# Kernel tuning notes

Measured on AMD Instinct MI355X. Metric: run time of the kernel, lower is better.

The kernel has to match this reference:

```python
import jax, jax.numpy as jnp
import numpy as np

B, L, H, P = 4, 4096, 1024, 256


def _bin_op(ei, ej):
    A_i, Bu_i = ei
    A_j, Bu_j = ej
    return (A_j * A_i, A_j * Bu_i + Bu_j)


def _s5(x, log_real, imag, B_real, B_imag, C_real, C_imag, D, log_Delta):
    Lam = jax.lax.complex(-jnp.exp(log_real), imag)                 # [P]
    B_tilde = jax.lax.complex(B_real, B_imag)                        # [P,H]
    C_tilde = jax.lax.complex(C_real, C_imag)                        # [H,P]
    Delta = jnp.exp(log_Delta)                                       # [P]
    Lambda_bar = jnp.exp(Lam * Delta)                                # [P]
    Lam_safe = jnp.where(jnp.abs(Lam) < 1e-6,
                         jnp.full_like(Lam, 1e-6), Lam)
    B_bar = ((Lambda_bar - 1.0) / Lam_safe)[:, None] * B_tilde       # [P,H]
    Bu = x.astype(jnp.complex64) @ B_bar.T                           # [B,L,P]
    La = jnp.broadcast_to(Lambda_bar[None, None, :], Bu.shape)
    _, xs = jax.lax.associative_scan(_bin_op, (La, Bu), axis=1)      # [B,L,P]
    ys = jnp.real(xs @ C_tilde.T) + D * x                            # [B,L,H]
    return jax.nn.gelu(ys, approximate=False)


def setup_inputs() -> dict:
    key = jax.random.key(0)
    ks = jax.random.split(key, 17)
    std_b = 1.0 / H ** 0.5
    std_c = 1.0 / P ** 0.5
    d = {"x": jax.random.normal(ks[0], (B, L, H), dtype=jnp.float32)}
    for i, pfx in enumerate(["fwd", "bwd"]):
        o = 1 + 8 * i
        d[pfx + "_log_real"] = jax.random.normal(ks[o], (P,)) * 0.5
        d[pfx + "_imag"] = jax.random.normal(ks[o + 1], (P,))
        d[pfx + "_B_real"] = jax.random.normal(ks[o + 2], (P, H)) * std_b
        d[pfx + "_B_imag"] = jax.random.normal(ks[o + 3], (P, H)) * std_b
        d[pfx + "_C_real"] = jax.random.normal(ks[o + 4], (H, P)) * std_c
        d[pfx + "_C_imag"] = jax.random.normal(ks[o + 5], (H, P)) * std_c
        d[pfx + "_D"] = jnp.ones((H,), dtype=jnp.float32)
        d[pfx + "_log_Delta"] = jnp.zeros((P,), dtype=jnp.float32)
    return d


def reference(x,
              fwd_log_real, fwd_imag, fwd_B_real, fwd_B_imag,
              fwd_C_real, fwd_C_imag, fwd_D, fwd_log_Delta,
              bwd_log_real, bwd_imag, bwd_B_real, bwd_B_imag,
              bwd_C_real, bwd_C_imag, bwd_D, bwd_log_Delta):
    y_f = _s5(x, fwd_log_real, fwd_imag, fwd_B_real, fwd_B_imag,
              fwd_C_real, fwd_C_imag, fwd_D, fwd_log_Delta)
    x_flip = jnp.flip(x, axis=1)
    y_b = _s5(x_flip, bwd_log_real, bwd_imag, bwd_B_real, bwd_B_imag,
              bwd_C_real, bwd_C_imag, bwd_D, bwd_log_Delta)
    return y_f + jnp.flip(y_b, axis=1)
```

## Files before the change

### kernel.cpp

```cpp
#include <hip/hip_runtime.h>
#include <math.h>


typedef short bf16x8 __attribute__((ext_vector_type(8)));
typedef float f32x4 __attribute__((ext_vector_type(4)));
typedef unsigned short u16x8 __attribute__((ext_vector_type(8)));

__device__ __forceinline__ unsigned short f2bf(float f) {
  union { float f; unsigned int u; } v; v.f = f;
  unsigned int r = (v.u + 0x7FFFu + ((v.u >> 16) & 1u)) >> 16;
  return (unsigned short)r;
}
__device__ __forceinline__ float bf2f(unsigned short s) {
  union { unsigned int u; float f; } v; v.u = ((unsigned int)s) << 16;
  return v.f;
}
__device__ __forceinline__ float gelu_fast(float v) {
  const float u = 1.5957691216057308f * fmaf(0.044715f * v, v * v, v);
  return v / (1.f + __expf(-u));
}
__device__ __forceinline__ void gload16(const unsigned short* g, void* l) {
  __builtin_amdgcn_global_load_lds(
      (const __attribute__((address_space(1))) void*)g,
      (__attribute__((address_space(3))) void*)l, 16, 0, 0);
}

__global__ __launch_bounds__(256) void cast_prep_kernel(
    const float* __restrict__ x, unsigned short* __restrict__ xbf,
    const float* __restrict__ flr, const float* __restrict__ fim,
    const float* __restrict__ fBr, const float* __restrict__ fBi,
    const float* __restrict__ fCr, const float* __restrict__ fCi,
    const float* __restrict__ flD,
    const float* __restrict__ blr, const float* __restrict__ bim,
    const float* __restrict__ bBr, const float* __restrict__ bBi,
    const float* __restrict__ bCr, const float* __restrict__ bCi,
    const float* __restrict__ blD,
    unsigned short* __restrict__ W, unsigned short* __restrict__ CmT,
    float4* __restrict__ lamp) {
  const int tid = threadIdx.x;
  if (blockIdx.x < 8192) {
    const size_t i = (size_t)blockIdx.x * 256 + tid;
    const float4* xv = (const float4*)x;
    float4 a = xv[2 * i], b = xv[2 * i + 1];
    u16x8 r;
    r[0] = f2bf(a.x); r[1] = f2bf(a.y); r[2] = f2bf(a.z); r[3] = f2bf(a.w);
    r[4] = f2bf(b.x); r[5] = f2bf(b.y); r[6] = f2bf(b.z); r[7] = f2bf(b.w);
    *(u16x8*)(xbf + 8 * i) = r;
    return;
  }
  const int bid = blockIdx.x - 8192;
  if (bid < 512) {
    const int dir = bid >> 8, p = bid & 255;
    const float* lr_ = dir ? blr : flr;
    const float* im_ = dir ? bim : fim;
    const float* lD_ = dir ? blD : flD;
    const float* Br_ = dir ? bBr : fBr;
    const float* Bi_ = dir ? bBi : fBi;
    const float Lre = -expf(lr_[p]);
    const float Lim = im_[p];
    const float Dl = expf(lD_[p]);
    const float ar = Lre * Dl, ai = Lim * Dl;
    const float er = expf(ar);
    const float lre = er * cosf(ai), lim = er * sinf(ai);
    const float e64 = expf(64.f * ar);
    const float l64re = e64 * cosf(64.f * ai), l64im = e64 * sinf(64.f * ai);
    float sre = Lre, sim = Lim;
    if (sqrtf(Lre * Lre + Lim * Lim) < 1e-6f) { sre = 1e-6f; sim = 0.f; }
    const float den = sre * sre + sim * sim;
    const float fre = ((lre - 1.f) * sre + lim * sim) / den;
    const float fi2 = (lim * sre - (lre - 1.f) * sim) / den;
    if (tid == 0) lamp[dir * 256 + p] = make_float4(lre, lim, l64re, l64im);
    const size_t rowR = (size_t)(dir * 512 + 2 * p) * 1024;
    const size_t rowI = rowR + 1024;
    for (int h = tid; h < 1024; h += 256) {
      const float Br = Br_[p * 1024 + h], Bi = Bi_[p * 1024 + h];
      W[rowR + h] = f2bf(fre * Br - fi2 * Bi);
      W[rowI + h] = f2bf(fre * Bi + fi2 * Br);
    }
  } else {
    const int h = bid - 512;
    for (int k = tid; k < 1024; k += 256) {
      const int dir = k >> 9, within = k & 511;
      const int p = within >> 1, comp = within & 1;
      const float* C = comp ? (dir ? bCi : fCi) : (dir ? bCr : fCr);
      float v = C[(size_t)h * 256 + p];
      if (comp) v = -v;
      CmT[(size_t)h * 1024 + k] = f2bf(v);
    }
  }
}

#define G256_STAGE(BUF, KT, APTR, BPTR)                                        \
  {                                                                            \
    const int k0 = (KT) << 6;                                                  \
    _Pragma("unroll") for (int i = 0; i < 4; ++i) {                            \
      const int r = (i << 6) + tr;                                             \
      const int o = ((BUF) << 15) + (i << 13) + (tid << 4);                    \
      gload16(APTR + (size_t)(m0 + r) * 1024 + (k0 + csw), (char*)As + o);     \
      gload16(BPTR + (size_t)(n0 + r) * 1024 + (k0 + csw), (char*)Bs + o);     \
    }                                                                          \
  }

#define PIPE_PUBLISH8()                                                        \
  asm volatile("s_waitcnt vmcnt(8)" ::: "memory");                             \
  __builtin_amdgcn_sched_barrier(0);                                           \
  __builtin_amdgcn_s_barrier();                                                \
  __builtin_amdgcn_sched_barrier(0);

#define PIPE_CLOSE()                                                           \
  __builtin_amdgcn_sched_barrier(0);                                           \
  __builtin_amdgcn_s_barrier();                                                \
  __builtin_amdgcn_sched_barrier(0);

#define G1_COMPUTE(BUF, ACC)                                                   \
  {                                                                            \
    const int bo = (BUF) << 14;                            \
    bf16x8 bF[4][2];                                                           \
    _Pragma("unroll") for (int n4 = 0; n4 < 4; ++n4)                           \
        _Pragma("unroll") for (int kk2 = 0; kk2 < 2; ++kk2) {                  \
      const int row = (wn << 6) + (n4 << 4) + fr;                              \
      bF[n4][kk2] =                                                            \
          *(const bf16x8*)&Bs[bo + row * 64 + (((kk2 << 5) + ks) ^ sw)];       \
    }                                                                          \
    _Pragma("unroll") for (int ph = 0; ph < 4; ++ph) {                         \
      bf16x8 aF[2][2];                                                         \
      _Pragma("unroll") for (int mf2 = 0; mf2 < 2; ++mf2)                      \
          _Pragma("unroll") for (int kk2 = 0; kk2 < 2; ++kk2) {                \
        const int row = (wm << 7) + (((ph << 1) + mf2) << 4) + fr;             \
        aF[mf2][kk2] =                                                         \
            *(const bf16x8*)&As[bo + row * 64 + (((kk2 << 5) + ks) ^ sw)];     \
      }                                                                        \
      __builtin_amdgcn_s_setprio(1);                                           \
      _Pragma("unroll") for (int mf2 = 0; mf2 < 2; ++mf2)                      \
          _Pragma("unroll") for (int n4 = 0; n4 < 4; ++n4)                     \
              _Pragma("unroll") for (int kk2 = 0; kk2 < 2; ++kk2)              \
                  ACC[(ph << 1) + mf2][n4] =                                   \
                      __builtin_amdgcn_mfma_f32_16x16x32_bf16(                 \
                          aF[mf2][kk2], bF[n4][kk2], ACC[(ph << 1) + mf2][n4], \
                          0, 0, 0);                                            \
      __builtin_amdgcn_s_setprio(0);                                           \
    }                                                                          \
  }

__global__ __launch_bounds__(512, 2) void gemm1_kernel(
    const unsigned short* __restrict__ xbf, const unsigned short* __restrict__ W,
    unsigned short* __restrict__ Zb) {
  __shared__ unsigned short As[2 * 256 * 64];
  __shared__ unsigned short Bs[2 * 256 * 64];
  const int tid = threadIdx.x;
  const int lane = tid & 63;
  const int w = tid >> 6;
  const int wm = w >> 2, wn = w & 3;
  const int fr = lane & 15;
  const int ks = (lane >> 4) << 3;
  const int sw = (fr & 7) << 3;
  const int tr = tid >> 3;
  const int csw = ((tid & 7) ^ (tr & 7)) << 3;
  const int bsw = ((blockIdx.x & 7) << 5) + (blockIdx.x >> 3);
  const int nt = bsw & 3, mt = bsw >> 2;
  const int m0 = mt << 8, n0 = nt << 8;

  f32x4 acc[8][4] = {};

  G256_STAGE(0, 0, xbf, W);
  int cur = 0;
  for (int kt = 0; kt < 15; ++kt) {
    G256_STAGE(cur ^ 1, kt + 1, xbf, W);
    PIPE_PUBLISH8();
    G1_COMPUTE(cur, acc);
    PIPE_CLOSE();
    cur ^= 1;
  }
  __syncthreads();
  G1_COMPUTE(cur, acc);

  const int rb = (lane >> 4) << 2;
#pragma unroll
  for (int mf = 0; mf < 8; ++mf)
#pragma unroll
    for (int n4 = 0; n4 < 4; ++n4) {
      const size_t gn = n0 + (wn << 6) + (n4 << 4) + fr;
#pragma unroll
      for (int r = 0; r < 4; ++r) {
        const size_t gm = m0 + (wm << 7) + (mf << 4) + rb + r;
        Zb[gm * 1024 + gn] = f2bf(acc[mf][n4][r]);
      }
    }
}

__global__ __launch_bounds__(256) void scanP_kernel(
    const unsigned int* __restrict__ Zp, const float4* __restrict__ lamp,
    float2* __restrict__ part) {
  const int p = threadIdx.x;
  const int k = blockIdx.x & 63;
  const int s = blockIdx.x >> 6;
  const int dir = s & 1, b = s >> 1;
  const float4 lp = lamp[dir * 256 + p];
  const float lre = lp.x, lim = lp.y;
  const size_t col = (size_t)dir * 256 + p;
  const size_t mbase = (size_t)b * 4096 + (size_t)k * 64;
  float sre = 0.f, sim = 0.f;
  if (dir == 0) {
    for (int i = 0; i < 64; ++i) {
      const unsigned int u = Zp[(mbase + i) * 512 + col];
      const float nr = fmaf(lre, sre, fmaf(-lim, sim, bf2f((unsigned short)u)));
      const float ni = fmaf(lre, sim, fmaf(lim, sre, bf2f((unsigned short)(u >> 16))));
      sre = nr; sim = ni;
    }
  } else {
    for (int i = 63; i >= 0; --i) {
      const unsigned int u = Zp[(mbase + i) * 512 + col];
      const float nr = fmaf(lre, sre, fmaf(-lim, sim, bf2f((unsigned short)u)));
      const float ni = fmaf(lre, sim, fmaf(lim, sre, bf2f((unsigned short)(u >> 16))));
      sre = nr; sim = ni;
    }
  }
  part[(size_t)(s * 64 + k) * 256 + p] = make_float2(sre, sim);
}

__global__ __launch_bounds__(256) void scanF_kernel(
    const unsigned int* __restrict__ Zp, const float4* __restrict__ lamp,
    const float2* __restrict__ part, unsigned int* __restrict__ xsbf) {
  const int p = threadIdx.x;
  const int k = blockIdx.x & 63;
  const int s = blockIdx.x >> 6;
  const int dir = s & 1, b = s >> 1;
  const float4 lp = lamp[dir * 256 + p];
  const float lre = lp.x, lim = lp.y, wr64 = lp.z, wi64 = lp.w;
  const size_t col = (size_t)dir * 256 + p;
  const size_t mbase = (size_t)b * 4096 + (size_t)k * 64;

  float cr = 0.f, ci = 0.f, wr = 1.f, wi = 0.f;
  if (dir == 0) {
    for (int j = k - 1; j >= 0; --j) {
      const float2 S = part[(size_t)(s * 64 + j) * 256 + p];
      cr = fmaf(wr, S.x, fmaf(-wi, S.y, cr));
      ci = fmaf(wr, S.y, fmaf(wi, S.x, ci));
      const float t = wr * wr64 - wi * wi64;
      wi = wr * wi64 + wi * wr64; wr = t;
    }
  } else {
    for (int j = k + 1; j < 64; ++j) {
      const float2 S = part[(size_t)(s * 64 + j) * 256 + p];
      cr = fmaf(wr, S.x, fmaf(-wi, S.y, cr));
      ci = fmaf(wr, S.y, fmaf(wi, S.x, ci));
      const float t = wr * wr64 - wi * wi64;
      wi = wr * wi64 + wi * wr64; wr = t;
    }
  }

  float sre = cr, sim = ci;
  if (dir == 0) {
    for (int i = 0; i < 64; ++i) {
      const size_t idx = (mbase + i) * 512 + col;
      const unsigned int u = Zp[idx];
      const float nr = fmaf(lre, sre, fmaf(-lim, sim, bf2f((unsigned short)u)));
      const float ni = fmaf(lre, sim, fmaf(lim, sre, bf2f((unsigned short)(u >> 16))));
      sre = nr; sim = ni;
      xsbf[idx] = (unsigned int)f2bf(sre) | ((unsigned int)f2bf(sim) << 16);
    }
  } else {
    for (int i = 63; i >= 0; --i) {
      const size_t idx = (mbase + i) * 512 + col;
      const unsigned int u = Zp[idx];
      const float nr = fmaf(lre, sre, fmaf(-lim, sim, bf2f((unsigned short)u)));
      const float ni = fmaf(lre, sim, fmaf(lim, sre, bf2f((unsigned short)(u >> 16))));
      sre = nr; sim = ni;
      xsbf[idx] = (unsigned int)f2bf(sre) | ((unsigned int)f2bf(sim) << 16);
    }
  }
}

#define GEMM_STAGE(BUF, KT, APTR, BPTR)                                        \
  {                                                                            \
    const int k0 = (KT) << 6;                                                  \
    _Pragma("unroll") for (int i = 0; i < 4; ++i) {                            \
      const int r = (i << 5) + tr;                                             \
      const int o = ((BUF) << 14) + (i << 12) + (tid << 4);                    \
      gload16(APTR + (size_t)(m0 + r) * 1024 + (k0 + csw), (char*)As + o);     \
      gload16(BPTR + (size_t)(n0 + r) * 1024 + (k0 + csw), (char*)Bs + o);     \
    }                                                                          \
  }

#define GEMM_COMPUTE(BUF, ACC)                                                 \
  {                                                                            \
    const int bo = (BUF) << 13;               \
    _Pragma("unroll") for (int kk = 0; kk < 64; kk += 32) {                    \
      bf16x8 af[4], bf_[4];                                                    \
      _Pragma("unroll") for (int m4 = 0; m4 < 4; ++m4) {                       \
        const int row = (wm << 6) + (m4 << 4) + fr;                            \
        af[m4] = *(const bf16x8*)&As[bo + row * 64 + ((kk + ks) ^ sw)];        \
      }                                                                        \
      _Pragma("unroll") for (int n4 = 0; n4 < 4; ++n4) {                       \
        const int row = (wn << 6) + (n4 << 4) + fr;                            \
        bf_[n4] = *(const bf16x8*)&Bs[bo + row * 64 + ((kk + ks) ^ sw)];       \
      }                                                                        \
      _Pragma("unroll") for (int m4 = 0; m4 < 4; ++m4)                         \
          _Pragma("unroll") for (int n4 = 0; n4 < 4; ++n4)                     \
              ACC[m4][n4] = __builtin_amdgcn_mfma_f32_16x16x32_bf16(           \
                  af[m4], bf_[n4], ACC[m4][n4], 0, 0, 0);                      \
    }                                                                          \
  }

__global__ __launch_bounds__(256, 2) void gemm2_kernel(
    const unsigned short* __restrict__ A2, const unsigned short* __restrict__ CmT,
    const unsigned short* __restrict__ xbf, const float* __restrict__ Df,
    const float* __restrict__ Db, float* __restrict__ out) {
  __shared__ unsigned short As[2 * 128 * 64];
  __shared__ unsigned short Bs[2 * 128 * 64];
  const int tid = threadIdx.x;
  const int lane = tid & 63;
  const int w = tid >> 6;
  const int wm = w >> 1, wn = w & 1;
  const int fr = lane & 15;
  const int ks = (lane >> 4) << 3;
  const int sw = (fr & 7) << 3;
  const int tr = tid >> 3;
  const int csw = ((tid & 7) ^ (tr & 7)) << 3;
  const int bsw = ((blockIdx.x & 7) << 7) + (blockIdx.x >> 3);
  const int nt = bsw & 7, mt = bsw >> 3;
  const int m0 = mt << 7, n0 = nt << 7;

  f32x4 accf[4][4] = {};
  f32x4 accb[4][4] = {};

  GEMM_STAGE(0, 0, A2, CmT);
  int cur = 0;
#pragma unroll
  for (int kt = 0; kt < 8; ++kt) {
    GEMM_STAGE(cur ^ 1, kt + 1, A2, CmT);
    PIPE_PUBLISH8();
    GEMM_COMPUTE(cur, accf);
    PIPE_CLOSE();
    cur ^= 1;
  }
#pragma unroll
  for (int kt = 8; kt < 15; ++kt) {
    GEMM_STAGE(cur ^ 1, kt + 1, A2, CmT);
    PIPE_PUBLISH8();
    GEMM_COMPUTE(cur, accb);
    PIPE_CLOSE();
    cur ^= 1;
  }
  __syncthreads();
  GEMM_COMPUTE(cur, accb);

  const int rb = (lane >> 4) << 2;
#pragma unroll
  for (int n4 = 0; n4 < 4; ++n4) {
    const size_t gn = n0 + (wn << 6) + (n4 << 4) + fr;
    const float dfv = Df[gn], dbv = Db[gn];
#pragma unroll
    for (int m4 = 0; m4 < 4; ++m4) {
#pragma unroll
      for (int r = 0; r < 4; ++r) {
        const size_t gm = m0 + (wm << 6) + (m4 << 4) + rb + r;
        const float xv = bf2f(xbf[gm * 1024 + gn]);
        out[gm * 1024 + gn] = gelu_fast(accf[m4][n4][r] + dfv * xv) +
                              gelu_fast(accb[m4][n4][r] + dbv * xv);
      }
    }
  }
}

extern "C" void kernel_launch(void* const* d_in, const int* in_sizes, int n_in,
                              void* d_out, int out_size, void* d_ws, size_t ws_size,
                              hipStream_t stream) {
  const float* x = (const float*)d_in[0];
  const float* flr = (const float*)d_in[1];
  const float* fim = (const float*)d_in[2];
  const float* fBr = (const float*)d_in[3];
  const float* fBi = (const float*)d_in[4];
  const float* fCr = (const float*)d_in[5];
  const float* fCi = (const float*)d_in[6];
  const float* fD  = (const float*)d_in[7];
  const float* flD = (const float*)d_in[8];
  const float* blr = (const float*)d_in[9];
  const float* bim = (const float*)d_in[10];
  const float* bBr = (const float*)d_in[11];
  const float* bBi = (const float*)d_in[12];
  const float* bCr = (const float*)d_in[13];
  const float* bCi = (const float*)d_in[14];
  const float* bD  = (const float*)d_in[15];
  const float* blD = (const float*)d_in[16];

  char* ws = (char*)d_ws;
  unsigned short* xbf  = (unsigned short*)(ws);
  unsigned short* W    = (unsigned short*)(ws + 33554432);
  unsigned short* CmT  = (unsigned short*)(ws + 35651584);
  unsigned short* Zb   = (unsigned short*)(ws + 37748736);
  unsigned short* xsbf = (unsigned short*)(ws + 71303168);
  float4*         lamp = (float4*)(ws + 104857600);
  float2*         part = (float2*)(ws + 104865792);

  cast_prep_kernel<<<9728, 256, 0, stream>>>(
      x, xbf, flr, fim, fBr, fBi, fCr, fCi, flD,
      blr, bim, bBr, bBi, bCr, bCi, blD, W, CmT, lamp);
  gemm1_kernel<<<256, 512, 0, stream>>>(xbf, W, Zb);
  scanP_kernel<<<512, 256, 0, stream>>>((unsigned int*)Zb, lamp, part);
  scanF_kernel<<<512, 256, 0, stream>>>((unsigned int*)Zb, lamp, part,
                                        (unsigned int*)xsbf);
  gemm2_kernel<<<1024, 256, 0, stream>>>(xsbf, CmT, xbf, fD, bD, (float*)d_out);
}
```

Measured before the change: 145.4 us.

## Fuse chunk-local scan into GEMM1 epilogue and simplify scan fixup pass

Result: faster. 135.1 us, median of 2 (-7.1%).

```diff
diff --git a/kernel.cpp b/kernel.cpp
--- a/kernel.cpp
+++ b/kernel.cpp
@@ -144,9 +144,11 @@
 
 __global__ __launch_bounds__(512, 2) void gemm1_kernel(
     const unsigned short* __restrict__ xbf, const unsigned short* __restrict__ W,
-    unsigned short* __restrict__ Zb) {
-  __shared__ unsigned short As[2 * 256 * 64];
-  __shared__ unsigned short Bs[2 * 256 * 64];
+    unsigned int* __restrict__ Zp, const float4* __restrict__ lamp,
+    float2* __restrict__ part) {
+  __shared__ unsigned short LDS[4 * 256 * 64];
+  unsigned short* As = LDS;
+  unsigned short* Bs = LDS + 2 * 256 * 64;
   const int tid = threadIdx.x;
   const int lane = tid & 63;
   const int w = tid >> 6;
@@ -159,6 +161,7 @@
   const int bsw = ((blockIdx.x & 7) << 5) + (blockIdx.x >> 3);
   const int nt = bsw & 3, mt = bsw >> 2;
   const int m0 = mt << 8, n0 = nt << 8;
+  const int rb = (lane >> 4) << 2;
 
   f32x4 acc[8][4] = {};
 
@@ -174,48 +177,54 @@
   __syncthreads();
   G1_COMPUTE(cur, acc);
 
-  const int rb = (lane >> 4) << 2;
+  __syncthreads();
+  unsigned short (*SB)[256] = (unsigned short(*)[256])LDS;
 #pragma unroll
   for (int mf = 0; mf < 8; ++mf)
 #pragma unroll
     for (int n4 = 0; n4 < 4; ++n4) {
-      const size_t gn = n0 + (wn << 6) + (n4 << 4) + fr;
+      const int lc = (wn << 6) + (n4 << 4) + fr;
 #pragma unroll
       for (int r = 0; r < 4; ++r) {
-        const size_t gm = m0 + (wm << 7) + (mf << 4) + rb + r;
-        Zb[gm * 1024 + gn] = f2bf(acc[mf][n4][r]);
+        const int lr = (wm << 7) + (mf << 4) + rb + r;
+        SB[lr][lc] = f2bf(acc[mf][n4][r]);
       }
     }
-}
-
-__global__ __launch_bounds__(256) void scanP_kernel(
-    const unsigned int* __restrict__ Zp, const float4* __restrict__ lamp,
-    float2* __restrict__ part) {
-  const int p = threadIdx.x;
-  const int k = blockIdx.x & 63;
-  const int s = blockIdx.x >> 6;
-  const int dir = s & 1, b = s >> 1;
-  const float4 lp = lamp[dir * 256 + p];
+  __syncthreads();
+
+  const int pp = tid & 127;
+  const int ch = tid >> 7;
+  const int gcp = (n0 >> 1) + pp;
+  const int sdir = gcp >> 8;
+  const int p = gcp & 255;
+  const float4 lp = lamp[sdir * 256 + p];
   const float lre = lp.x, lim = lp.y;
-  const size_t col = (size_t)dir * 256 + p;
-  const size_t mbase = (size_t)b * 4096 + (size_t)k * 64;
+  const unsigned int* SBu = (const unsigned int*)LDS;
+  const size_t growbase = (size_t)(m0 + (ch << 6));
   float sre = 0.f, sim = 0.f;
-  if (dir == 0) {
+  if (sdir == 0) {
     for (int i = 0; i < 64; ++i) {
-      const unsigned int u = Zp[(mbase + i) * 512 + col];
+      const unsigned int u = SBu[((ch << 6) + i) * 128 + pp];
       const float nr = fmaf(lre, sre, fmaf(-lim, sim, bf2f((unsigned short)u)));
       const float ni = fmaf(lre, sim, fmaf(lim, sre, bf2f((unsigned short)(u >> 16))));
       sre = nr; sim = ni;
+      Zp[(growbase + i) * 512 + gcp] =
+          (unsigned int)f2bf(sre) | ((unsigned int)f2bf(sim) << 16);
     }
   } else {
     for (int i = 63; i >= 0; --i) {
-      const unsigned int u = Zp[(mbase + i) * 512 + col];
+      const unsigned int u = SBu[((ch << 6) + i) * 128 + pp];
       const float nr = fmaf(lre, sre, fmaf(-lim, sim, bf2f((unsigned short)u)));
       const float ni = fmaf(lre, sim, fmaf(lim, sre, bf2f((unsigned short)(u >> 16))));
       sre = nr; sim = ni;
-    }
-  }
-  part[(size_t)(s * 64 + k) * 256 + p] = make_float2(sre, sim);
+      Zp[(growbase + i) * 512 + gcp] =
+          (unsigned int)f2bf(sre) | ((unsigned int)f2bf(sim) << 16);
+    }
+  }
+  const int b = m0 >> 12;
+  const int kchunk = ((m0 & 4095) >> 6) + ch;
+  const int s = b * 2 + sdir;
+  part[(size_t)(s * 64 + kchunk) * 256 + p] = make_float2(sre, sim);
 }
 
 __global__ __launch_bounds__(256) void scanF_kernel(
@@ -249,24 +258,27 @@
     }
   }
 
-  float sre = cr, sim = ci;
+  float qr = lre * cr - lim * ci;
+  float qi = lre * ci + lim * cr;
   if (dir == 0) {
     for (int i = 0; i < 64; ++i) {
       const size_t idx = (mbase + i) * 512 + col;
       const unsigned int u = Zp[idx];
-      const float nr = fmaf(lre, sre, fmaf(-lim, sim, bf2f((unsigned short)u)));
-      const float ni = fmaf(lre, sim, fmaf(lim, sre, bf2f((unsigned short)(u >> 16))));
-      sre = nr; sim = ni;
-      xsbf[idx] = (unsigned int)f2bf(sre) | ((unsigned int)f2bf(sim) << 16);
+      const float vr = bf2f((unsigned short)u) + qr;
+      const float vi = bf2f((unsigned short)(u >> 16)) + qi;
+      xsbf[idx] = (unsigned int)f2bf(vr) | ((unsigned int)f2bf(vi) << 16);
+      const float t = lre * qr - lim * qi;
+      qi = lre * qi + lim * qr; qr = t;
     }
   } else {
     for (int i = 63; i >= 0; --i) {
       const size_t idx = (mbase + i) * 512 + col;
       const unsigned int u = Zp[idx];
-      const float nr = fmaf(lre, sre, fmaf(-lim, sim, bf2f((unsigned short)u)));
-      const float ni = fmaf(lre, sim, fmaf(lim, sre, bf2f((unsigned short)(u >> 16))));
-      sre = nr; sim = ni;
-      xsbf[idx] = (unsigned int)f2bf(sre) | ((unsigned int)f2bf(sim) << 16);
+      const float vr = bf2f((unsigned short)u) + qr;
+      const float vi = bf2f((unsigned short)(u >> 16)) + qi;
+      xsbf[idx] = (unsigned int)f2bf(vr) | ((unsigned int)f2bf(vi) << 16);
+      const float t = lre * qr - lim * qi;
+      qi = lre * qi + lim * qr; qr = t;
     }
   }
 }
@@ -275,7 +287,7 @@
   {                                                                            \
     const int k0 = (KT) << 6;                                                  \
     _Pragma("unroll") for (int i = 0; i < 4; ++i) {                            \
-      const int r = (i << 5) + tr;                                             \
+      const int r = (i << 5) + tr2;                                            \
       const int o = ((BUF) << 14) + (i << 12) + (tid << 4);                    \
       gload16(APTR + (size_t)(m0 + r) * 1024 + (k0 + csw), (char*)As + o);     \
       gload16(BPTR + (size_t)(n0 + r) * 1024 + (k0 + csw), (char*)Bs + o);     \
@@ -315,8 +327,8 @@
   const int fr = lane & 15;
   const int ks = (lane >> 4) << 3;
   const int sw = (fr & 7) << 3;
-  const int tr = tid >> 3;
-  const int csw = ((tid & 7) ^ (tr & 7)) << 3;
+  const int tr2 = tid >> 3;
+  const int csw = ((tid & 7) ^ (tr2 & 7)) << 3;
   const int bsw = ((blockIdx.x & 7) << 7) + (blockIdx.x >> 3);
   const int nt = bsw & 7, mt = bsw >> 3;
   const int m0 = mt << 7, n0 = nt << 7;
@@ -396,8 +408,7 @@
   cast_prep_kernel<<<9728, 256, 0, stream>>>(
       x, xbf, flr, fim, fBr, fBi, fCr, fCi, flD,
       blr, bim, bBr, bBi, bCr, bCi, blD, W, CmT, lamp);
-  gemm1_kernel<<<256, 512, 0, stream>>>(xbf, W, Zb);
-  scanP_kernel<<<512, 256, 0, stream>>>((unsigned int*)Zb, lamp, part);
+  gemm1_kernel<<<256, 512, 0, stream>>>(xbf, W, (unsigned int*)Zb, lamp, part);
   scanF_kernel<<<512, 256, 0, stream>>>((unsigned int*)Zb, lamp, part,
                                         (unsigned int*)xsbf);
   gemm2_kernel<<<1024, 256, 0, stream>>>(xsbf, CmT, xbf, fD, bD, (float*)d_out);
```
